# Performance work log

Measured on AMD Instinct MI355X. Metric: run time of the kernel, lower is better.

## Reference

```python
import jax, jax.numpy as jnp
import numpy as np

D_MODEL = 2048
NUM_HEADS = 16
D_H = D_MODEL // NUM_HEADS
D_LATENT = 512
B, S = 2, 2048


def setup_inputs() -> dict:
    key = jax.random.key(0)
    ks = jax.random.split(key, 10)
    sd = lambda fan_in: 1.0 / np.sqrt(fan_in)
    x = jax.random.normal(ks[0], (B, S, D_MODEL), dtype=jnp.float32)
    # weights stored as [in, out] so y = x @ W + b (same math as nn.Linear)
    w_latent = jax.random.uniform(ks[1], (D_MODEL, D_LATENT), jnp.float32, -sd(D_MODEL), sd(D_MODEL))
    b_latent = jax.random.uniform(ks[2], (D_LATENT,), jnp.float32, -sd(D_MODEL), sd(D_MODEL))
    w_q = jax.random.uniform(ks[3], (D_MODEL, D_MODEL), jnp.float32, -sd(D_MODEL), sd(D_MODEL))
    b_q = jax.random.uniform(ks[4], (D_MODEL,), jnp.float32, -sd(D_MODEL), sd(D_MODEL))
    # per-head K/V projections batched into [H, d_latent, d_h]
    w_k = jax.random.uniform(ks[5], (NUM_HEADS, D_LATENT, D_H), jnp.float32, -sd(D_LATENT), sd(D_LATENT))
    b_k = jax.random.uniform(ks[6], (NUM_HEADS, D_H), jnp.float32, -sd(D_LATENT), sd(D_LATENT))
    w_v = jax.random.uniform(ks[7], (NUM_HEADS, D_LATENT, D_H), jnp.float32, -sd(D_LATENT), sd(D_LATENT))
    b_v = jax.random.uniform(ks[8], (NUM_HEADS, D_H), jnp.float32, -sd(D_LATENT), sd(D_LATENT))
    w_o = jax.random.uniform(ks[9], (D_MODEL, D_MODEL), jnp.float32, -sd(D_MODEL), sd(D_MODEL))
    b_o = jnp.zeros((D_MODEL,), jnp.float32)
    return {"x": x, "w_latent": w_latent, "b_latent": b_latent, "w_q": w_q, "b_q": b_q,
            "w_k": w_k, "b_k": b_k, "w_v": w_v, "b_v": b_v, "w_o": w_o, "b_o": b_o}


def reference(x, w_latent, b_latent, w_q, b_q, w_k, b_k, w_v, b_v, w_o, b_o):
    batch, seq, d = x.shape
    # latent KV compression: [B,S,d_latent]
    z = x @ w_latent + b_latent
    # queries: [B,H,S,d_h]
    q = (x @ w_q + b_q).reshape(batch, seq, NUM_HEADS, D_H).transpose(0, 2, 1, 3)
    # per-head K/V projections fused into one batched GEMM: [B,H,S,d_h]
    k = jnp.einsum('bsl,hld->bhsd', z, w_k) + b_k[None, :, None, :]
    v = jnp.einsum('bsl,hld->bhsd', z, w_v) + b_v[None, :, None, :]
    attn = jnp.einsum('bhqd,bhkd->bhqk', q, k) / np.sqrt(D_H).astype(np.float32)
    attn = jax.nn.softmax(attn, axis=-1)
    out = jnp.einsum('bhqk,bhkd->bhqd', attn, v)          # [B,H,S,d_h]
    out = out.transpose(0, 2, 1, 3).reshape(batch, seq, d)  # [B,S,D]
    return out @ w_o + b_o
```

## Files before the change

kernel.cpp:

```cpp
#include <hip/hip_runtime.h>
#include <hip/hip_bf16.h>

#define H_ATT   16
#define DH      128
#define DMODEL  2048
#define DLAT    512
#define NB      2
#define SEQ     2048
#define MROWS   (NB * SEQ)
#define NQZ     (DMODEL + DLAT)
#define NKV     (2 * DMODEL)

#define SCL2 0.12751744f

typedef __bf16          bf16x8_t __attribute__((ext_vector_type(8)));
typedef float           f32x4_t  __attribute__((ext_vector_type(4)));
typedef unsigned short  u16x4_t  __attribute__((ext_vector_type(4)));

#if __has_builtin(__builtin_amdgcn_exp2f)
#define EXP2F(x) __builtin_amdgcn_exp2f(x)
#else
#define EXP2F(x) exp2f(x)
#endif

__device__ __forceinline__ unsigned short f2bf_u16(float f) {
  union { __bf16 b; unsigned short u; } cv; cv.b = (__bf16)f; return cv.u;
}

__device__ __forceinline__ void async_copy16(const __bf16* g, __bf16* l) {
  __builtin_amdgcn_global_load_lds(
      (const __attribute__((address_space(1))) unsigned int*)g,
      (__attribute__((address_space(3))) unsigned int*)l, 16, 0, 0);
}

#define NB_CAST 8192
#define NB_WQ   4096
#define NB_WL   1024
#define NB_WK   1024
#define NB_WV   1024
#define NB_WO   4096
#define NB_BIAS 26
#define NB_PREP (NB_CAST + NB_WQ + NB_WL + NB_WK + NB_WV + NB_WO + NB_BIAS)

__global__ void prep(const float* __restrict__ x,
                     const float* __restrict__ w_q, const float* __restrict__ w_latent,
                     const float* __restrict__ w_k, const float* __restrict__ w_v,
                     const float* __restrict__ w_o,
                     const float* __restrict__ b_q, const float* __restrict__ b_lat,
                     const float* __restrict__ b_k, const float* __restrict__ b_v,
                     __bf16* __restrict__ xb, __bf16* __restrict__ wqzt,
                     __bf16* __restrict__ wkvt, __bf16* __restrict__ wot,
                     float* __restrict__ bqz, float* __restrict__ bkv) {
  __shared__ float tile[32][33];
  int bi = blockIdx.x;
  int t  = threadIdx.x;

  if (bi < NB_CAST) {
    int i = bi * 256 + t;
    float4 v = ((const float4*)x)[i];
    ushort4 o;
    o.x = f2bf_u16(v.x); o.y = f2bf_u16(v.y); o.z = f2bf_u16(v.z); o.w = f2bf_u16(v.w);
    ((ushort4*)xb)[i] = o;
    return;
  }
  bi -= NB_CAST;

  const float* in = nullptr; __bf16* out = nullptr;
  int R = 0, C = 0, bx = 0, by = 0; float scale = 1.f;
  if (bi < NB_WQ) {
    in = w_q; out = wqzt; R = DMODEL; C = DMODEL; scale = SCL2;
    bx = bi & 63; by = bi >> 6;
  } else if ((bi -= NB_WQ) < NB_WL) {
    in = w_latent; out = wqzt + (size_t)DMODEL * DMODEL; R = DMODEL; C = DLAT;
    bx = bi & 15; by = bi >> 4;
  } else if ((bi -= NB_WL) < NB_WK) {
    int h = bi >> 6, rem = bi & 63;
    in = w_k + (size_t)h * DLAT * DH; out = wkvt + (size_t)h * DH * DLAT;
    R = DLAT; C = DH; bx = rem & 3; by = rem >> 2;
  } else if ((bi -= NB_WK) < NB_WV) {
    int h = bi >> 6, rem = bi & 63;
    in = w_v + (size_t)h * DLAT * DH;
    out = wkvt + (size_t)DMODEL * DLAT + (size_t)h * DH * DLAT;
    R = DLAT; C = DH; bx = rem & 3; by = rem >> 2;
  } else if ((bi -= NB_WV) < NB_WO) {
    in = w_o; out = wot; R = DMODEL; C = DMODEL;
    bx = bi & 63; by = bi >> 6;
  } else {
    bi -= NB_WO;
    int idx = bi * 256 + t;
    if (idx < DMODEL)                bqz[idx] = b_q[idx] * SCL2;
    else if (idx < NQZ)              bqz[idx] = b_lat[idx - DMODEL];
    else if (idx < NQZ + DMODEL)     bkv[idx - NQZ] = b_k[idx - NQZ];
    else if (idx < NQZ + NKV)        bkv[idx - NQZ] = b_v[idx - NQZ - DMODEL];
    return;
  }

  int tx = t & 31, ty = t >> 5;
  const float* ip = in + (size_t)(by * 32) * C + bx * 32;
  #pragma unroll
  for (int i = 0; i < 4; ++i)
    tile[ty + i * 8][tx] = ip[(size_t)(ty + i * 8) * C + tx];
  __syncthreads();
  __bf16* op = out + (size_t)(bx * 32) * R + by * 32;
  #pragma unroll
  for (int i = 0; i < 4; ++i)
    op[(size_t)(ty + i * 8) * R + tx] = (__bf16)(tile[tx][ty + i * 8] * scale);
}

#define BM 128
#define BN 128
#define BK 32

__device__ __forceinline__ void storec(float*  p, float v) { *p = v; }
__device__ __forceinline__ void storec(__bf16* p, float v) { *p = (__bf16)v; }

template <typename OutT, bool KVDUAL>
__global__ __launch_bounds__(256, 3)
void gemm_bt(const __bf16* __restrict__ A, const __bf16* __restrict__ Bt,
             const float* __restrict__ bias, OutT* __restrict__ C,
             __bf16* __restrict__ Cvt,
             int M, int N, int K, int lda, int ldc) {
  __shared__ __align__(16) __bf16 As[2][BM * BK];
  __shared__ __align__(16) __bf16 Bs[2][BN * BK];
  const int t    = threadIdx.x;
  const int wave = t >> 6, lane = t & 63;
  const int quad = lane >> 4, l16 = lane & 15;
  const int wm = (wave >> 1) * 64, wn = (wave & 1) * 64;
  const int row0 = blockIdx.y * BM, col0 = blockIdx.x * BN;
  const int srow = t >> 2, skc = t & 3;

  const __bf16* Ag  = A  + (size_t)(row0 + srow)      * lda + skc * 8;
  const __bf16* Ag2 = A  + (size_t)(row0 + srow + 64) * lda + skc * 8;
  const __bf16* Bg  = Bt + (size_t)(col0 + srow)      * K   + skc * 8;
  const __bf16* Bg2 = Bt + (size_t)(col0 + srow + 64) * K   + skc * 8;

  auto stage = [&](int k0, int buf) {
    async_copy16(Ag  + k0, As[buf] + t * 8);
    async_copy16(Ag2 + k0, As[buf] + 2048 + t * 8);
    async_copy16(Bg  + k0, Bs[buf] + t * 8);
    async_copy16(Bg2 + k0, Bs[buf] + 2048 + t * 8);
  };

  f32x4_t acc[4][4] = {};

  stage(0, 0);
  __syncthreads();

  for (int k0 = 0, kb = 0; k0 < K; k0 += BK, ++kb) {
    const int cur = kb & 1;
    if (k0 + BK < K) stage(k0 + BK, cur ^ 1);

    bf16x8_t af[4], bfr[4];
    #pragma unroll
    for (int i = 0; i < 4; ++i)
      af[i] = *(const bf16x8_t*)(As[cur] + (wm + i * 16 + l16) * BK + quad * 8);
    #pragma unroll
    for (int j = 0; j < 4; ++j)
      bfr[j] = *(const bf16x8_t*)(Bs[cur] + (wn + j * 16 + l16) * BK + quad * 8);
    #pragma unroll
    for (int i = 0; i < 4; ++i)
      #pragma unroll
      for (int j = 0; j < 4; ++j)
        acc[i][j] = __builtin_amdgcn_mfma_f32_16x16x32_bf16(af[i], bfr[j], acc[i][j], 0, 0, 0);

    __syncthreads();
  }

  const bool vmode = KVDUAL && (col0 >= DMODEL);
  #pragma unroll
  for (int j = 0; j < 4; ++j) {
    int col = col0 + wn + j * 16 + l16;
    float bj = bias[col];
    #pragma unroll
    for (int i = 0; i < 4; ++i) {
      int row = row0 + wm + i * 16 + quad * 4;
      if (vmode) {
        u16x4_t pw;
        #pragma unroll
        for (int r = 0; r < 4; ++r) pw[r] = f2bf_u16(acc[i][j][r] + bj);
        size_t bb = (size_t)(row >> 11);
        int s = row & (SEQ - 1);
        *(u16x4_t*)(Cvt + bb * ((size_t)DMODEL * SEQ) + (size_t)(col - DMODEL) * SEQ + s) = pw;
      } else {
        #pragma unroll
        for (int r = 0; r < 4; ++r)
          storec(&C[(size_t)(row + r) * ldc + col], acc[i][j][r] + bj);
      }
    }
  }
}

#define TQ 128
#define TK 64
#define NT (SEQ / TK)

__global__ __launch_bounds__(256, 2)
void mla_attn(const __bf16* __restrict__ Qm, const __bf16* __restrict__ Km,
              const __bf16* __restrict__ Vtg, __bf16* __restrict__ Om) {
  __shared__ __align__(16) __bf16 smem[5 * 16 * 512];
  __bf16* const Kls = smem;
  __bf16* const Vls = smem + 2 * (16 * 512);
  __bf16* const Ps  = smem + 4 * (16 * 512);
  float*  const Lbuf = (float*)smem;

  const int t    = threadIdx.x;
  const int wave = t >> 6, lane = t & 63;
  const int quad = lane >> 4, l16 = lane & 15;
  const int wq = wave >> 1, wk = wave & 1, wd = wave & 1;
  const int lin  = blockIdx.x;
  const int xcd  = lin & 7, slot = lin >> 3;
  const int hb   = xcd * 4 + (slot >> 4);
  const int b    = hb >> 4, h = hb & 15;
  const int q0   = (slot & 15) * TQ;
  const size_t kbase  = (size_t)b * SEQ * DMODEL + (size_t)h * DH;
  const size_t vtbase = ((size_t)b * DMODEL + (size_t)h * DH) * SEQ;
  const size_t obase  = (size_t)b * SEQ * DMODEL + (size_t)h * DH;

  bf16x8_t qf[4][4];
  #pragma unroll
  for (int nt = 0; nt < 4; ++nt) {
    const __bf16* qp = Qm + ((size_t)b * SEQ + q0 + wq * 64 + nt * 16 + l16) * NQZ
                       + (size_t)h * DH + quad * 8;
    #pragma unroll
    for (int kc = 0; kc < 4; ++kc)
      qf[nt][kc] = *(const bf16x8_t*)(qp + kc * 32);
  }

  auto stageK = [&](int kt0, int buf) {
    #pragma unroll
    for (int i2 = 0; i2 < 4; ++i2) {
      int bidx = wave * 4 + i2;
      int mt = bidx >> 2, kc = bidx & 3;
      async_copy16(Km + kbase + (size_t)(kt0 + mt * 16 + l16) * DMODEL + kc * 32 + quad * 8,
                   Kls + buf * (16 * 512) + bidx * 512 + lane * 8);
    }
  };
  auto stageV = [&](int kt0, int buf) {
    #pragma unroll
    for (int i2 = 0; i2 < 4; ++i2) {
      int bidx = wave * 4 + i2;
      int dt = bidx >> 1, ks = bidx & 1;
      async_copy16(Vtg + vtbase + (size_t)(dt * 16 + l16) * SEQ + kt0 + ks * 32 + quad * 8,
                   Vls + buf * (16 * 512) + bidx * 512 + lane * 8);
    }
  };

  f32x4_t acc_o[4][4] = {};
  float l_part[4] = {0.f, 0.f, 0.f, 0.f};

  stageK(0, 0);
  stageV(0, 0);

  f32x4_t acc_s[2][4];
  for (int it = 0; it < NT; ++it) {
    __syncthreads();

    if (it + 1 < NT) stageK((it + 1) * TK, (it + 1) & 1);

    if (it > 0) {
      const __bf16* Vb = Vls + ((it - 1) & 1) * (16 * 512);
      __builtin_amdgcn_s_setprio(1);
      #pragma unroll
      for (int ks = 0; ks < 2; ++ks) {
        bf16x8_t pf[4];
        #pragma unroll
        for (int mq = 0; mq < 4; ++mq)
          pf[mq] = *(const bf16x8_t*)(Ps + ((wq * 4 + mq) * 2 + ks) * 512 + lane * 8);
        #pragma unroll
        for (int nd = 0; nd < 4; ++nd) {
          bf16x8_t vf = *(const bf16x8_t*)(Vb + ((wd * 4 + nd) * 2 + ks) * 512 + lane * 8);
          #pragma unroll
          for (int mq = 0; mq < 4; ++mq)
            acc_o[mq][nd] = __builtin_amdgcn_mfma_f32_16x16x32_bf16(pf[mq], vf, acc_o[mq][nd], 0, 0, 0);
        }
      }
      __builtin_amdgcn_s_setprio(0);
    }

    #pragma unroll
    for (int mtl = 0; mtl < 2; ++mtl)
      #pragma unroll
      for (int nt = 0; nt < 4; ++nt)
        acc_s[mtl][nt] = f32x4_t{0.f, 0.f, 0.f, 0.f};
    const __bf16* Kb = Kls + (it & 1) * (16 * 512);
    __builtin_amdgcn_s_setprio(1);
    #pragma unroll
    for (int kc = 0; kc < 4; ++kc)
      #pragma unroll
      for (int mtl = 0; mtl < 2; ++mtl) {
        bf16x8_t kf = *(const bf16x8_t*)(Kb + ((wk * 2 + mtl) * 4 + kc) * 512 + lane * 8);
        #pragma unroll
        for (int nt = 0; nt < 4; ++nt)
          acc_s[mtl][nt] = __builtin_amdgcn_mfma_f32_16x16x32_bf16(kf, qf[nt][kc], acc_s[mtl][nt], 0, 0, 0);
      }
    __builtin_amdgcn_s_setprio(0);

    __builtin_amdgcn_s_barrier();

    if (it + 1 < NT) stageV((it + 1) * TK, (it + 1) & 1);

    #pragma unroll
    for (int nt = 0; nt < 4; ++nt) {
      #pragma unroll
      for (int mtl = 0; mtl < 2; ++mtl) {
        u16x4_t pw;
        float s = 0.f;
        #pragma unroll
        for (int r = 0; r < 4; ++r) {
          float p = EXP2F(fminf(acc_s[mtl][nt][r], 80.f));
          s += p;
          pw[r] = f2bf_u16(p);
        }
        l_part[nt] += s;
        *(u16x4_t*)(Ps + ((wq * 4 + nt) * 2 + wk) * 512
                    + ((mtl * 2 + (quad >> 1)) * 16 + l16) * 8 + (quad & 1) * 4) = pw;
      }
    }
  }

  __syncthreads();
  {
    const __bf16* Vb = Vls + ((NT - 1) & 1) * (16 * 512);
    __builtin_amdgcn_s_setprio(1);
    #pragma unroll
    for (int ks = 0; ks < 2; ++ks) {
      bf16x8_t pf[4];
      #pragma unroll
      for (int mq = 0; mq < 4; ++mq)
        pf[mq] = *(const bf16x8_t*)(Ps + ((wq * 4 + mq) * 2 + ks) * 512 + lane * 8);
      #pragma unroll
      for (int nd = 0; nd < 4; ++nd) {
        bf16x8_t vf = *(const bf16x8_t*)(Vb + ((wd * 4 + nd) * 2 + ks) * 512 + lane * 8);
        #pragma unroll
        for (int mq = 0; mq < 4; ++mq)
          acc_o[mq][nd] = __builtin_amdgcn_mfma_f32_16x16x32_bf16(pf[mq], vf, acc_o[mq][nd], 0, 0, 0);
      }
    }
    __builtin_amdgcn_s_setprio(0);
  }

  #pragma unroll
  for (int nt = 0; nt < 4; ++nt) {
    float lp = l_part[nt];
    lp += __shfl_xor(lp, 16);
    lp += __shfl_xor(lp, 32);
    Lbuf[wk * TQ + wq * 64 + nt * 16 + l16] = lp;
  }
  __syncthreads();
  #pragma unroll
  for (int mq = 0; mq < 4; ++mq) {
    float li[4];
    #pragma unroll
    for (int r = 0; r < 4; ++r) {
      int qq = wq * 64 + mq * 16 + quad * 4 + r;
      li[r] = 1.f / (Lbuf[0 * TQ + qq] + Lbuf[1 * TQ + qq]);
    }
    #pragma unroll
    for (int nd = 0; nd < 4; ++nd) {
      int col = wd * 64 + nd * 16 + l16;
      #pragma unroll
      for (int r = 0; r < 4; ++r) {
        int row = q0 + wq * 64 + mq * 16 + quad * 4 + r;
        Om[obase + (size_t)row * DMODEL + col] = (__bf16)(acc_o[mq][nd][r] * li[r]);
      }
    }
  }
}

extern "C" void kernel_launch(void* const* d_in, const int* in_sizes, int n_in,
                              void* d_out, int out_size, void* d_ws, size_t ws_size,
                              hipStream_t stream) {
  (void)in_sizes; (void)n_in; (void)out_size; (void)ws_size;
  const float* x        = (const float*)d_in[0];
  const float* w_latent = (const float*)d_in[1];
  const float* b_latent = (const float*)d_in[2];
  const float* w_q      = (const float*)d_in[3];
  const float* b_q      = (const float*)d_in[4];
  const float* w_k      = (const float*)d_in[5];
  const float* b_k      = (const float*)d_in[6];
  const float* w_v      = (const float*)d_in[7];
  const float* b_v      = (const float*)d_in[8];
  const float* w_o      = (const float*)d_in[9];
  const float* b_o      = (const float*)d_in[10];
  float* out = (float*)d_out;

  __bf16* ws = (__bf16*)d_ws;
  __bf16* xb   = ws; ws += (size_t)MROWS * DMODEL;
  __bf16* wqzt = ws; ws += (size_t)NQZ * DMODEL;
  __bf16* wkvt = ws; ws += (size_t)NKV * DLAT;
  __bf16* wot  = ws; ws += (size_t)DMODEL * DMODEL;
  __bf16* qzb  = ws; ws += (size_t)MROWS * NQZ;
  __bf16* kb   = ws; ws += (size_t)MROWS * DMODEL;
  __bf16* vt   = ws; ws += (size_t)MROWS * DMODEL;
  __bf16* ao   = ws; ws += (size_t)MROWS * DMODEL;
  float*  bqz  = (float*)ws;
  float*  bkv  = bqz + NQZ;

  dim3 blk256(256);
  prep<<<NB_PREP, blk256, 0, stream>>>(x, w_q, w_latent, w_k, w_v, w_o,
                                       b_q, b_latent, b_k, b_v,
                                       xb, wqzt, wkvt, wot, bqz, bkv);

  gemm_bt<__bf16, false><<<dim3(NQZ/BN, MROWS/BM), blk256, 0, stream>>>(
      xb, wqzt, bqz, qzb, nullptr, MROWS, NQZ, DMODEL, DMODEL, NQZ);
  gemm_bt<__bf16, true><<<dim3(NKV/BN, MROWS/BM), blk256, 0, stream>>>(
      qzb + DMODEL, wkvt, bkv, kb, vt, MROWS, NKV, DLAT, NQZ, DMODEL);

  mla_attn<<<dim3(512), blk256, 0, stream>>>(qzb, kb, vt, ao);

  gemm_bt<float, false><<<dim3(DMODEL/BN, MROWS/BM), blk256, 0, stream>>>(
      ao, wot, b_o, out, nullptr, MROWS, DMODEL, DMODEL, DMODEL, DMODEL);
}
```

Before: 341.1 us.

## Remap GEMM blocks across XCDs and stage transposed V epilogue through LDS

Block indices are remapped so that consecutive linear block IDs, which are dispatched round-robin across the 8 XCDs, give each XCD a contiguous set of row tiles, aiming to improve L2 reuse of the A operand. The V-transpose epilogue now writes the tile to shared memory first and then stores 16-byte contiguous chunks along the sequence dimension, replacing the scattered 8-byte column stores. The remap hardcodes the assumption that the grid's y dimension is 32 row tiles and that the total block count is a multiple of 8, so it is incorrect for other grid shapes. It also adds two barriers per phase in the epilogue.

```diff
diff --git a/kernel.cpp b/kernel.cpp
--- a/kernel.cpp
+++ b/kernel.cpp
@@ -120,25 +120,31 @@
              const float* __restrict__ bias, OutT* __restrict__ C,
              __bf16* __restrict__ Cvt,
              int M, int N, int K, int lda, int ldc) {
-  __shared__ __align__(16) __bf16 As[2][BM * BK];
-  __shared__ __align__(16) __bf16 Bs[2][BN * BK];
+  __shared__ __align__(16) __bf16 smem[16384];
   const int t    = threadIdx.x;
   const int wave = t >> 6, lane = t & 63;
   const int quad = lane >> 4, l16 = lane & 15;
   const int wm = (wave >> 1) * 64, wn = (wave & 1) * 64;
-  const int row0 = blockIdx.y * BM, col0 = blockIdx.x * BN;
+
+  const int gx  = gridDim.x;
+  const int lin = blockIdx.y * gx + blockIdx.x;
+  const int xcd = lin & 7, slot = lin >> 3;
+  const int bxi = slot >> 2, byi = xcd * 4 + (slot & 3);
+  const int row0 = byi * BM, col0 = bxi * BN;
+
   const int srow = t >> 2, skc = t & 3;
-
   const __bf16* Ag  = A  + (size_t)(row0 + srow)      * lda + skc * 8;
   const __bf16* Ag2 = A  + (size_t)(row0 + srow + 64) * lda + skc * 8;
   const __bf16* Bg  = Bt + (size_t)(col0 + srow)      * K   + skc * 8;
   const __bf16* Bg2 = Bt + (size_t)(col0 + srow + 64) * K   + skc * 8;
 
   auto stage = [&](int k0, int buf) {
-    async_copy16(Ag  + k0, As[buf] + t * 8);
-    async_copy16(Ag2 + k0, As[buf] + 2048 + t * 8);
-    async_copy16(Bg  + k0, Bs[buf] + t * 8);
-    async_copy16(Bg2 + k0, Bs[buf] + 2048 + t * 8);
+    __bf16* Asb = smem + buf * 4096;
+    __bf16* Bsb = smem + 8192 + buf * 4096;
+    async_copy16(Ag  + k0, Asb + t * 8);
+    async_copy16(Ag2 + k0, Asb + 2048 + t * 8);
+    async_copy16(Bg  + k0, Bsb + t * 8);
+    async_copy16(Bg2 + k0, Bsb + 2048 + t * 8);
   };
 
   f32x4_t acc[4][4] = {};
@@ -150,13 +156,15 @@
     const int cur = kb & 1;
     if (k0 + BK < K) stage(k0 + BK, cur ^ 1);
 
+    const __bf16* Asb = smem + cur * 4096;
+    const __bf16* Bsb = smem + 8192 + cur * 4096;
     bf16x8_t af[4], bfr[4];
     #pragma unroll
     for (int i = 0; i < 4; ++i)
-      af[i] = *(const bf16x8_t*)(As[cur] + (wm + i * 16 + l16) * BK + quad * 8);
+      af[i] = *(const bf16x8_t*)(Asb + (wm + i * 16 + l16) * BK + quad * 8);
     #pragma unroll
     for (int j = 0; j < 4; ++j)
-      bfr[j] = *(const bf16x8_t*)(Bs[cur] + (wn + j * 16 + l16) * BK + quad * 8);
+      bfr[j] = *(const bf16x8_t*)(Bsb + (wn + j * 16 + l16) * BK + quad * 8);
     #pragma unroll
     for (int i = 0; i < 4; ++i)
       #pragma unroll
@@ -167,21 +175,47 @@
   }
 
   const bool vmode = KVDUAL && (col0 >= DMODEL);
-  #pragma unroll
-  for (int j = 0; j < 4; ++j) {
-    int col = col0 + wn + j * 16 + l16;
-    float bj = bias[col];
-    #pragma unroll
-    for (int i = 0; i < 4; ++i) {
-      int row = row0 + wm + i * 16 + quad * 4;
-      if (vmode) {
-        u16x4_t pw;
-        #pragma unroll
-        for (int r = 0; r < 4; ++r) pw[r] = f2bf_u16(acc[i][j][r] + bj);
-        size_t bb = (size_t)(row >> 11);
-        int s = row & (SEQ - 1);
-        *(u16x4_t*)(Cvt + bb * ((size_t)DMODEL * SEQ) + (size_t)(col - DMODEL) * SEQ + s) = pw;
-      } else {
+  if (vmode) {
+    __bf16* T = smem;
+    const int cl = t >> 2, qk = t & 3;
+    const size_t bb = (size_t)(row0 >> 11);
+    const int s0 = row0 & (SEQ - 1);
+    #pragma unroll
+    for (int ph = 0; ph < 2; ++ph) {
+      if ((wave & 1) == ph) {
+        #pragma unroll
+        for (int j = 0; j < 4; ++j) {
+          int c = j * 16 + l16;
+          float bj = bias[col0 + ph * 64 + c];
+          #pragma unroll
+          for (int i = 0; i < 4; ++i) {
+            int r = wm + i * 16 + quad * 4;
+            u16x4_t pw;
+            #pragma unroll
+            for (int rr = 0; rr < 4; ++rr) pw[rr] = f2bf_u16(acc[i][j][rr] + bj);
+            *(u16x4_t*)(T + c * 136 + r) = pw;
+          }
+        }
+      }
+      __syncthreads();
+      {
+        int colg = col0 - DMODEL + ph * 64 + cl;
+        __bf16* dst = Cvt + bb * ((size_t)DMODEL * SEQ) + (size_t)colg * SEQ + s0 + qk * 32;
+        const __bf16* src = T + cl * 136 + qk * 32;
+        #pragma unroll
+        for (int m = 0; m < 4; ++m)
+          *(bf16x8_t*)(dst + m * 8) = *(const bf16x8_t*)(src + m * 8);
+      }
+      __syncthreads();
+    }
+  } else {
+    #pragma unroll
+    for (int j = 0; j < 4; ++j) {
+      int col = col0 + wn + j * 16 + l16;
+      float bj = bias[col];
+      #pragma unroll
+      for (int i = 0; i < 4; ++i) {
+        int row = row0 + wm + i * 16 + quad * 4;
         #pragma unroll
         for (int r = 0; r < 4; ++r)
           storec(&C[(size_t)(row + r) * ldc + col], acc[i][j][r] + bj);
```

Result: faster. 330.3 us (-3.2%).
